# Performance work log

Hardware: AMD Instinct MI355X
Metric: run time of the kernel (lower is better)

The kernel has to match this reference:

```python
import jax, jax.numpy as jnp
import numpy as np

B, S, D = 8, 2048, 1024


def setup_inputs() -> dict:
    key = jax.random.key(0)
    k1, k2, k3, k4 = jax.random.split(key, 4)
    scale = 1.0 / np.sqrt(D)
    x = jax.random.normal(k1, (B, S, D), dtype=jnp.float32)
    Wq = jax.random.normal(k2, (D, D), dtype=jnp.float32) * scale
    Wk = jax.random.normal(k3, (D, D), dtype=jnp.float32) * scale
    Wv = jax.random.normal(k4, (D, D), dtype=jnp.float32) * scale
    return {"x": x, "Wq": Wq, "Wk": Wk, "Wv": Wv}


def reference(x, Wq, Wk, Wv):
    # nn.Linear(d, d, bias=False): y = x @ W.T
    q = jnp.einsum('bsd,ed->bse', x, Wq)
    k = jnp.einsum('bsd,ed->bse', x, Wk)
    v = jnp.einsum('bsd,ed->bse', x, Wv)
    S_len = x.shape[1]
    d_k = k.shape[-1]
    # full score matrix, causal mask (strict upper triangle -> -inf)
    scores = jnp.einsum('bqd,bkd->bqk', q, k)
    causal = jnp.triu(jnp.ones((S_len, S_len), dtype=bool), k=1)
    scores = jnp.where(causal[None, :, :], -jnp.inf, scores)
    attn = jax.nn.softmax(scores / jnp.sqrt(jnp.asarray(d_k, scores.dtype)), axis=-1)
    # dropout p=0.0 (eval) -> identity
    return jnp.einsum('bqk,bkd->bqd', attn, v)
```

## Files before the change

kernel.cpp:

```cpp
#include <hip/hip_runtime.h>


typedef _Float16 v8h __attribute__((ext_vector_type(8)));
typedef _Float16 v4h __attribute__((ext_vector_type(4)));
typedef float    v4f __attribute__((ext_vector_type(4)));

#define BM 256
#define BN 256

__device__ __forceinline__ void async16(const _Float16* g, _Float16* l) {
  __builtin_amdgcn_global_load_lds(
      (__attribute__((address_space(1))) void*)(void*)g,
      (__attribute__((address_space(3))) void*)l, 16, 0, 0);
}

__device__ __forceinline__ void rd_a(const _Float16* U, int offA0, int base,
                                     v8h a[4]) {
#pragma unroll
  for (int i = 0; i < 4; ++i) a[i] = *(const v8h*)(U + offA0 + (base + i) * 512);
}
__device__ __forceinline__ void rd_b(const _Float16* U, int offB0, v8h b[4]) {
#pragma unroll
  for (int j = 0; j < 4; ++j) b[j] = *(const v8h*)(U + offB0 + j * 512);
}

__device__ __forceinline__ void mfma16(const v8h a[4], const v8h b[4],
                                       v4f (*accr)[4]) {
  __builtin_amdgcn_s_setprio(1);
#pragma unroll
  for (int i = 0; i < 4; ++i)
#pragma unroll
    for (int j = 0; j < 4; ++j)
      accr[i][j] = __builtin_amdgcn_mfma_f32_16x16x32_f16(a[i], b[j],
                                                          accr[i][j], 0, 0, 0);
  __builtin_amdgcn_s_setprio(0);
}

#define VM8 asm volatile("s_waitcnt vmcnt(8)" ::: "memory")
#define VM4 asm volatile("s_waitcnt vmcnt(4)" ::: "memory")
#define VM0 asm volatile("s_waitcnt vmcnt(0)" ::: "memory")
#define LG8                                                                  \
  asm volatile("s_waitcnt lgkmcnt(8)" ::: "memory");                         \
  __builtin_amdgcn_sched_barrier(0)
#define LG4                                                                  \
  asm volatile("s_waitcnt lgkmcnt(4)" ::: "memory");                         \
  __builtin_amdgcn_sched_barrier(0)
#define LG0                                                                  \
  asm volatile("s_waitcnt lgkmcnt(0)" ::: "memory");                         \
  __builtin_amdgcn_sched_barrier(0)
#define BAR __builtin_amdgcn_s_barrier()

__device__ __forceinline__ void gemm_loop(const _Float16* Ab, int lda,
                                          const _Float16* Bb, int ldb,
                                          int NKT, _Float16* lds,
                                          int w, int lane, int wr, int wc,
                                          int lr, int quad, v4f acc[8][4]) {
  const int offA0 = (wr + lr) * 32 + ((quad ^ (((wr + lr) >> 1) & 3)) * 8);
  const int offB0 = 8192 + (wc + lr) * 32 + ((quad ^ (((wc + lr) >> 1) & 3)) * 8);

  const int u0 = w * 128 + lane;
  const int u1 = u0 + 64;
  const int r0 = u0 >> 2, c0 = (u0 & 3) ^ ((r0 >> 1) & 3);
  const int r1 = u1 >> 2, c1 = (u1 & 3) ^ ((r1 >> 1) & 3);
  const _Float16* pA0 = Ab + (size_t)r0 * lda + c0 * 8;
  const _Float16* pA1 = Ab + (size_t)r1 * lda + c1 * 8;
  const _Float16* pB0 = Bb + (size_t)r0 * ldb + c0 * 8;
  const _Float16* pB1 = Bb + (size_t)r1 * ldb + c1 * 8;
  const int dA0 = (w * 128) * 8;
  const int dA1 = (w * 128 + 64) * 8;

#define STAGE(T)                                                             \
  do {                                                                       \
    _Float16* Ld = lds + ((T) & 3) * 16384;                                  \
    async16(pA0 + (T) * 32, Ld + dA0);                                       \
    async16(pB0 + (T) * 32, Ld + 8192 + dA0);                                \
    async16(pA1 + (T) * 32, Ld + dA1);                                       \
    async16(pB1 + (T) * 32, Ld + 8192 + dA1);                                \
  } while (0)
#define SL(T) (lds + ((T) & 3) * 16384)

  v8h aLo[4], aHi[4], bE[4], bO[4];

  STAGE(0);
  STAGE(1);
  STAGE(2);
  VM8;
  BAR;
  rd_a(SL(0), offA0, 0, aLo);
  rd_b(SL(0), offB0, bE);

  for (int t2 = 0; t2 < NKT - 4; t2 += 2) {
    VM8; BAR;
    rd_a(SL(t2), offA0, 4, aHi);
    STAGE(t2 + 3);
    LG4; mfma16(aLo, bE, &acc[0]);
    VM8; BAR;
    rd_a(SL(t2 + 1), offA0, 0, aLo);
    rd_b(SL(t2 + 1), offB0, bO);
    LG8; mfma16(aHi, bE, &acc[4]);
    VM8; BAR;
    rd_a(SL(t2 + 1), offA0, 4, aHi);
    STAGE(t2 + 4);
    LG4; mfma16(aLo, bO, &acc[0]);
    VM8; BAR;
    rd_a(SL(t2 + 2), offA0, 0, aLo);
    rd_b(SL(t2 + 2), offB0, bE);
    LG8; mfma16(aHi, bO, &acc[4]);
  }

  VM8; BAR;
  rd_a(SL(NKT - 4), offA0, 4, aHi);
  STAGE(NKT - 1);
  LG4; mfma16(aLo, bE, &acc[0]);
  VM8; BAR;
  rd_a(SL(NKT - 3), offA0, 0, aLo);
  rd_b(SL(NKT - 3), offB0, bO);
  LG8; mfma16(aHi, bE, &acc[4]);
  VM8; BAR;
  rd_a(SL(NKT - 3), offA0, 4, aHi);
  LG4; mfma16(aLo, bO, &acc[0]);
  VM4; BAR;
  rd_a(SL(NKT - 2), offA0, 0, aLo);
  rd_b(SL(NKT - 2), offB0, bE);
  LG8; mfma16(aHi, bO, &acc[4]);

  VM4; BAR;
  rd_a(SL(NKT - 2), offA0, 4, aHi);
  LG4; mfma16(aLo, bE, &acc[0]);
  VM0; BAR;
  rd_a(SL(NKT - 1), offA0, 0, aLo);
  rd_b(SL(NKT - 1), offB0, bO);
  LG8; mfma16(aHi, bE, &acc[4]);
  BAR;
  rd_a(SL(NKT - 1), offA0, 4, aHi);
  LG4; mfma16(aLo, bO, &acc[0]);
  LG0; mfma16(aHi, bO, &acc[4]);
#undef STAGE
#undef SL
}

__device__ __forceinline__ void grid_swz(int& bx, int& by) {
  const int gx = gridDim.x;
  const int n = gx * gridDim.y;
  const int f = blockIdx.x + blockIdx.y * gx;
  const int s = (f & 7) * (n >> 3) + (f >> 3);
  bx = s % gx;
  by = s / gx;
}

__global__ __launch_bounds__(256)
void cvt_f16(const float* __restrict__ src, _Float16* __restrict__ dst) {
  const int i = (blockIdx.x * 256 + threadIdx.x) * 8;
  float4 a = *(const float4*)(src + i);
  float4 b = *(const float4*)(src + i + 4);
  v8h o = {(_Float16)a.x, (_Float16)a.y, (_Float16)a.z, (_Float16)a.w,
           (_Float16)b.x, (_Float16)b.y, (_Float16)b.z, (_Float16)b.w};
  *(v8h*)(dst + i) = o;
}

__global__ __launch_bounds__(512, 2)
void proj_gemm(const _Float16* __restrict__ X, const _Float16* __restrict__ W,
               _Float16* __restrict__ Qb, _Float16* __restrict__ Kb,
               _Float16* __restrict__ Vt) {
  __shared__ _Float16 lds[65536];
  const int tid = threadIdx.x;
  int bx, by;
  grid_swz(bx, by);
  const int n0 = bx * BN, m0 = by * BM;
  const int which = n0 >> 10;
  const int nw = n0 & 1023;

  const int lane = tid & 63, w = tid >> 6;
  const int wr = (w >> 2) * 128, wc = (w & 3) * 64;
  const int lr = lane & 15, quad = lane >> 4;

  v4f acc[8][4];
#pragma unroll
  for (int i = 0; i < 8; ++i)
#pragma unroll
    for (int j = 0; j < 4; ++j) acc[i][j] = (v4f){0.f, 0.f, 0.f, 0.f};

  gemm_loop(X + (size_t)m0 * 1024, 1024, W + (size_t)n0 * 1024, 1024,
            32, lds, w, lane, wr, wc, lr, quad, acc);

#pragma unroll
  for (int i = 0; i < 8; ++i) {
    const int r0 = m0 + wr + i * 16 + quad * 4;
#pragma unroll
    for (int j = 0; j < 4; ++j) {
      const int cl = wc + j * 16 + lr;
      if (which < 2) {
        _Float16* dst = (which == 0) ? Qb : Kb;
        const int col = nw + cl;
#pragma unroll
        for (int rg = 0; rg < 4; ++rg)
          dst[(size_t)(r0 + rg) * 1024 + col] = (_Float16)acc[i][j][rg];
      } else {
        const int d = nw + cl;
        const int b = r0 >> 11, s = r0 & 2047;
        v4h o = {(_Float16)acc[i][j][0], (_Float16)acc[i][j][1],
                 (_Float16)acc[i][j][2], (_Float16)acc[i][j][3]};
        *(v4h*)(Vt + (size_t)b * 1024 * 2048 + (size_t)d * 2048 + s) = o;
      }
    }
  }
}

__global__ __launch_bounds__(512, 2)
void scores_gemm(const _Float16* __restrict__ Q, const _Float16* __restrict__ K,
                 _Float16* __restrict__ Sc) {
  __shared__ _Float16 lds[65536];
  const int tid = threadIdx.x;
  int bx, by;
  grid_swz(bx, by);
  const int bz = blockIdx.z;
  const int n0 = bx * BN, m0 = by * BM;
  _Float16* Cb = Sc + (size_t)bz * 2048 * 2048;

  if (bx > by) return;

  const _Float16* Qz = Q + (size_t)bz * 2048 * 1024;
  const _Float16* Kz = K + (size_t)bz * 2048 * 1024;

  const int lane = tid & 63, w = tid >> 6;
  const int wr = (w >> 2) * 128, wc = (w & 3) * 64;
  const int lr = lane & 15, quad = lane >> 4;

  v4f acc[8][4];
#pragma unroll
  for (int i = 0; i < 8; ++i)
#pragma unroll
    for (int j = 0; j < 4; ++j) acc[i][j] = (v4f){0.f, 0.f, 0.f, 0.f};

  gemm_loop(Qz + (size_t)m0 * 1024, 1024, Kz + (size_t)n0 * 1024, 1024,
            32, lds, w, lane, wr, wc, lr, quad, acc);

  const _Float16 ninf = (_Float16)(-__builtin_inff());
#pragma unroll
  for (int i = 0; i < 8; ++i) {
    const int r0 = m0 + wr + i * 16 + quad * 4;
#pragma unroll
    for (int j = 0; j < 4; ++j) {
      const int cc = n0 + wc + j * 16 + lr;
#pragma unroll
      for (int rg = 0; rg < 4; ++rg) {
        const int rr = r0 + rg;
        Cb[(size_t)rr * 2048 + cc] = (cc > rr) ? ninf : (_Float16)acc[i][j][rg];
      }
    }
  }
}

__global__ __launch_bounds__(256)
void softmax_rows(_Float16* __restrict__ Sc) {
  _Float16* base = Sc + (size_t)blockIdx.x * 2048;
  const int q = blockIdx.x & 2047;
  const int ktile = ((q >> 8) + 1) << 8;
  const int tid = threadIdx.x;
  const int lane = tid & 63, w = tid >> 6;
  const bool active = tid * 8 < ktile;

  float f[8];
  if (active) {
    v8h pv = *(const v8h*)(base + tid * 8);
#pragma unroll
    for (int j = 0; j < 8; ++j) f[j] = (float)pv[j];
  } else {
#pragma unroll
    for (int j = 0; j < 8; ++j) f[j] = -__builtin_inff();
  }

  float mx = f[0];
#pragma unroll
  for (int j = 1; j < 8; ++j) mx = fmaxf(mx, f[j]);
#pragma unroll
  for (int off = 32; off; off >>= 1) mx = fmaxf(mx, __shfl_xor(mx, off));
  __shared__ float redm[4], reds[4];
  if (lane == 0) redm[w] = mx;
  __syncthreads();
  mx = fmaxf(fmaxf(redm[0], redm[1]), fmaxf(redm[2], redm[3]));

  const float scale = 0.03125f;
  float e[8], s = 0.f;
#pragma unroll
  for (int j = 0; j < 8; ++j) {
    e[j] = __expf((f[j] - mx) * scale);
    s += e[j];
  }
#pragma unroll
  for (int off = 32; off; off >>= 1) s += __shfl_xor(s, off);
  if (lane == 0) reds[w] = s;
  __syncthreads();
  s = reds[0] + reds[1] + reds[2] + reds[3];
  const float inv = 1.0f / s;
  if (active) {
    v8h pv;
#pragma unroll
    for (int j = 0; j < 8; ++j) pv[j] = (_Float16)(e[j] * inv);
    *(v8h*)(base + tid * 8) = pv;
  }
}

__global__ __launch_bounds__(512, 2)
void pv_gemm(const _Float16* __restrict__ P, const _Float16* __restrict__ Vt,
             float* __restrict__ Out) {
  __shared__ _Float16 lds[65536];
  const int tid = threadIdx.x;
  int bx, by;
  grid_swz(bx, by);
  const int bz = blockIdx.z;
  const int n0 = bx * BN, m0 = by * BM;
  const _Float16* Pb = P + (size_t)bz * 2048 * 2048;
  const _Float16* Vb = Vt + (size_t)bz * 1024 * 2048;
  float* Cb = Out + (size_t)bz * 2048 * 1024;

  const int lane = tid & 63, w = tid >> 6;
  const int wr = (w >> 2) * 128, wc = (w & 3) * 64;
  const int lr = lane & 15, quad = lane >> 4;

  v4f acc[8][4];
#pragma unroll
  for (int i = 0; i < 8; ++i)
#pragma unroll
    for (int j = 0; j < 4; ++j) acc[i][j] = (v4f){0.f, 0.f, 0.f, 0.f};

  gemm_loop(Pb + (size_t)m0 * 2048, 2048, Vb + (size_t)n0 * 2048, 2048,
            (by + 1) * 8, lds, w, lane, wr, wc, lr, quad, acc);

#pragma unroll
  for (int i = 0; i < 8; ++i) {
    const int r0 = m0 + wr + i * 16 + quad * 4;
#pragma unroll
    for (int j = 0; j < 4; ++j) {
      const int cc = n0 + wc + j * 16 + lr;
#pragma unroll
      for (int rg = 0; rg < 4; ++rg)
        Cb[(size_t)(r0 + rg) * 1024 + cc] = acc[i][j][rg];
    }
  }
}

extern "C" void kernel_launch(void* const* d_in, const int* in_sizes, int n_in,
                              void* d_out, int out_size, void* d_ws, size_t ws_size,
                              hipStream_t stream) {
  const int B = 8, S = 2048, D = 1024;
  const int M = B * S;
  const float* x  = (const float*)d_in[0];
  const float* Wq = (const float*)d_in[1];
  const float* Wk = (const float*)d_in[2];
  const float* Wv = (const float*)d_in[3];
  float* out = (float*)d_out;

  char* ws = (char*)d_ws;
  _Float16* Qb = (_Float16*)ws;
  _Float16* Kb = (_Float16*)(ws + (size_t)33554432);
  _Float16* Vt = (_Float16*)(ws + (size_t)67108864);
  _Float16* Sc = (_Float16*)(ws + (size_t)100663296);
  _Float16* xh = Sc;
  _Float16* Wh = Sc + (size_t)M * D;

  cvt_f16<<<(M * D) / 2048, 256, 0, stream>>>(x, xh);
  cvt_f16<<<(D * D) / 2048, 256, 0, stream>>>(Wq, Wh);
  cvt_f16<<<(D * D) / 2048, 256, 0, stream>>>(Wk, Wh + (size_t)D * D);
  cvt_f16<<<(D * D) / 2048, 256, 0, stream>>>(Wv, Wh + (size_t)2 * D * D);

  proj_gemm<<<dim3(12, M / BM, 1), 512, 0, stream>>>(xh, Wh, Qb, Kb, Vt);

  scores_gemm<<<dim3(S / BN, S / BM, B), 512, 0, stream>>>(Qb, Kb, Sc);

  softmax_rows<<<B * S, 256, 0, stream>>>(Sc);

  pv_gemm<<<dim3(D / BN, S / BM, B), 512, 0, stream>>>(Sc, Vt, out);
}
```

Measured before the change: 397.1 us.

## Simplify GEMM main loop to a single-stage loop and merge weight conversions

Replaces the hand-tuned, ping-ponged GEMM inner loop (two B register sets, partial lgkmcnt waits, unrolled by two with an explicit epilogue) with a plain per-tile loop. The new loop waits for all LDS reads to finish and adds extra barriers before each MFMA block. It also merges the three weight fp32-to-fp16 conversion launches into one kernel to cut launch overhead. The simpler loop gives up overlap between LDS reads and MFMA work, so the GEMMs are likely to stall more.

```diff
diff --git a/kernel.cpp b/kernel.cpp
--- a/kernel.cpp
+++ b/kernel.cpp
@@ -39,12 +39,6 @@
 #define VM8 asm volatile("s_waitcnt vmcnt(8)" ::: "memory")
 #define VM4 asm volatile("s_waitcnt vmcnt(4)" ::: "memory")
 #define VM0 asm volatile("s_waitcnt vmcnt(0)" ::: "memory")
-#define LG8                                                                  \
-  asm volatile("s_waitcnt lgkmcnt(8)" ::: "memory");                         \
-  __builtin_amdgcn_sched_barrier(0)
-#define LG4                                                                  \
-  asm volatile("s_waitcnt lgkmcnt(4)" ::: "memory");                         \
-  __builtin_amdgcn_sched_barrier(0)
 #define LG0                                                                  \
   asm volatile("s_waitcnt lgkmcnt(0)" ::: "memory");                         \
   __builtin_amdgcn_sched_barrier(0)
@@ -79,62 +73,33 @@
   } while (0)
 #define SL(T) (lds + ((T) & 3) * 16384)
 
-  v8h aLo[4], aHi[4], bE[4], bO[4];
+  v8h aLo[4], aHi[4], bC[4];
 
   STAGE(0);
   STAGE(1);
   STAGE(2);
   VM8;
   BAR;
-  rd_a(SL(0), offA0, 0, aLo);
-  rd_b(SL(0), offB0, bE);
-
-  for (int t2 = 0; t2 < NKT - 4; t2 += 2) {
-    VM8; BAR;
-    rd_a(SL(t2), offA0, 4, aHi);
-    STAGE(t2 + 3);
-    LG4; mfma16(aLo, bE, &acc[0]);
-    VM8; BAR;
-    rd_a(SL(t2 + 1), offA0, 0, aLo);
-    rd_b(SL(t2 + 1), offB0, bO);
-    LG8; mfma16(aHi, bE, &acc[4]);
-    VM8; BAR;
-    rd_a(SL(t2 + 1), offA0, 4, aHi);
-    STAGE(t2 + 4);
-    LG4; mfma16(aLo, bO, &acc[0]);
-    VM8; BAR;
-    rd_a(SL(t2 + 2), offA0, 0, aLo);
-    rd_b(SL(t2 + 2), offB0, bE);
-    LG8; mfma16(aHi, bO, &acc[4]);
-  }
-
-  VM8; BAR;
-  rd_a(SL(NKT - 4), offA0, 4, aHi);
-  STAGE(NKT - 1);
-  LG4; mfma16(aLo, bE, &acc[0]);
-  VM8; BAR;
-  rd_a(SL(NKT - 3), offA0, 0, aLo);
-  rd_b(SL(NKT - 3), offB0, bO);
-  LG8; mfma16(aHi, bE, &acc[4]);
-  VM8; BAR;
-  rd_a(SL(NKT - 3), offA0, 4, aHi);
-  LG4; mfma16(aLo, bO, &acc[0]);
-  VM4; BAR;
-  rd_a(SL(NKT - 2), offA0, 0, aLo);
-  rd_b(SL(NKT - 2), offB0, bE);
-  LG8; mfma16(aHi, bO, &acc[4]);
-
-  VM4; BAR;
-  rd_a(SL(NKT - 2), offA0, 4, aHi);
-  LG4; mfma16(aLo, bE, &acc[0]);
-  VM0; BAR;
-  rd_a(SL(NKT - 1), offA0, 0, aLo);
-  rd_b(SL(NKT - 1), offB0, bO);
-  LG8; mfma16(aHi, bE, &acc[4]);
-  BAR;
-  rd_a(SL(NKT - 1), offA0, 4, aHi);
-  LG4; mfma16(aLo, bO, &acc[0]);
-  LG0; mfma16(aHi, bO, &acc[4]);
+
+  for (int t = 0; t < NKT; ++t) {
+    rd_a(SL(t), offA0, 0, aLo);
+    rd_b(SL(t), offB0, bC);
+    if (t + 3 < NKT) STAGE(t + 3);
+    BAR;
+    LG0;
+    mfma16(aLo, bC, &acc[0]);
+    BAR;
+    rd_a(SL(t), offA0, 4, aHi);
+    if (t <= NKT - 4) {
+      VM4;
+    } else if (t == NKT - 3) {
+      VM0;
+    }
+    BAR;
+    LG0;
+    mfma16(aHi, bC, &acc[4]);
+    BAR;
+  }
 #undef STAGE
 #undef SL
 }
@@ -156,6 +121,20 @@
   v8h o = {(_Float16)a.x, (_Float16)a.y, (_Float16)a.z, (_Float16)a.w,
            (_Float16)b.x, (_Float16)b.y, (_Float16)b.z, (_Float16)b.w};
   *(v8h*)(dst + i) = o;
+}
+
+__global__ __launch_bounds__(256)
+void cvt_f16_w(const float* __restrict__ Wq, const float* __restrict__ Wk,
+               const float* __restrict__ Wv, _Float16* __restrict__ dst) {
+  const int bid = blockIdx.x;
+  const int m = bid >> 9;
+  const float* src = (m == 0) ? Wq : (m == 1) ? Wk : Wv;
+  const int i = ((bid & 511) * 256 + threadIdx.x) * 8;
+  float4 a = *(const float4*)(src + i);
+  float4 b = *(const float4*)(src + i + 4);
+  v8h o = {(_Float16)a.x, (_Float16)a.y, (_Float16)a.z, (_Float16)a.w,
+           (_Float16)b.x, (_Float16)b.y, (_Float16)b.z, (_Float16)b.w};
+  *(v8h*)(dst + (size_t)m * 1048576 + i) = o;
 }
 
 __global__ __launch_bounds__(512, 2)
@@ -360,9 +339,7 @@
   _Float16* Wh = Sc + (size_t)M * D;
 
   cvt_f16<<<(M * D) / 2048, 256, 0, stream>>>(x, xh);
-  cvt_f16<<<(D * D) / 2048, 256, 0, stream>>>(Wq, Wh);
-  cvt_f16<<<(D * D) / 2048, 256, 0, stream>>>(Wk, Wh + (size_t)D * D);
-  cvt_f16<<<(D * D) / 2048, 256, 0, stream>>>(Wv, Wh + (size_t)2 * D * D);
+  cvt_f16_w<<<1536, 256, 0, stream>>>(Wq, Wk, Wv, Wh);
 
   proj_gemm<<<dim3(12, M / BM, 1), 512, 0, stream>>>(xh, Wh, Qb, Kb, Vt);
 
```

Result: no change. 393.6 us (-0.9%).
